# Performance work log

Hardware: AMD Instinct MI355X
Metric: run time of the kernel (lower is better)

## Reference

```python
import jax, jax.numpy as jnp
import numpy as np

B, S, D = 2, 2048, 2048
NQ, NKV = 32, 8
HD = D // NQ  # 64
THETA = 10000.0


def _rope_tables(seq_len, head_dim, theta):
    k = jnp.arange(0, head_dim, 2)[: head_dim // 2].astype(jnp.float32)
    inv_freq = 1.0 / (theta ** (k / head_dim))
    pos = jnp.arange(seq_len, dtype=jnp.float32)
    ang = pos[:, None] * inv_freq[None, :]          # [S, HD/2]
    ang = jnp.concatenate([ang, ang], axis=-1)       # [S, HD]
    return jnp.cos(ang), jnp.sin(ang)


def _apply_rope(x, cos, sin):
    # x: [B, H, S, HD]; cos/sin: [S, HD]
    h = x.shape[-1] // 2
    x1, x2 = x[..., :h], x[..., h:]
    rotated = jnp.concatenate([-x2, x1], axis=-1)
    return (x * cos[None, None] + rotated * sin[None, None]).astype(x.dtype)


def setup_inputs() -> dict:
    key = jax.random.key(0)
    ks = jax.random.split(key, 6)
    x = jax.random.normal(ks[0], (B, S, D), dtype=jnp.float32)
    attention_mask = jnp.ones((B, S), dtype=jnp.int32)
    Wq = jax.random.normal(ks[1], (NQ * HD, D), dtype=jnp.float32) * 0.02
    Wk = jax.random.normal(ks[2], (NKV * HD, D), dtype=jnp.float32) * 0.02
    Wv = jax.random.normal(ks[3], (NKV * HD, D), dtype=jnp.float32) * 0.02
    Wo = jax.random.normal(ks[4], (D, D), dtype=jnp.float32) * 0.02
    return {"x": x, "attention_mask": attention_mask,
            "Wq": Wq, "Wk": Wk, "Wv": Wv, "Wo": Wo}


def reference(x, attention_mask, Wq, Wk, Wv, Wo):
    b, s, d = x.shape
    # projections (nn.Linear: y = x @ W.T)
    q = jnp.einsum('bsd,od->bso', x, Wq).reshape(b, s, NQ, HD).transpose(0, 2, 1, 3)
    k = jnp.einsum('bsd,od->bso', x, Wk).reshape(b, s, NKV, HD).transpose(0, 2, 1, 3)
    v = jnp.einsum('bsd,od->bso', x, Wv).reshape(b, s, NKV, HD).transpose(0, 2, 1, 3)
    cos, sin = _rope_tables(s, HD, THETA)
    q = _apply_rope(q, cos, sin)
    k = _apply_rope(k, cos, sin)
    g = NQ // NKV
    k = jnp.repeat(k, g, axis=1)  # [b, NQ, s, HD]
    v = jnp.repeat(v, g, axis=1)
    attn = jnp.einsum('bhqd,bhkd->bhqk', q, k)
    causal = jnp.triu(jnp.ones((s, s), dtype=bool), k=1)
    attn = jnp.where(causal[None, None], -jnp.inf, attn)
    attn = jax.nn.softmax(attn / jnp.sqrt(jnp.float32(HD)), axis=-1)
    out = jnp.einsum('bhqk,bhkd->bhqd', attn, v)
    out = out.transpose(0, 2, 1, 3).reshape(b, s, d)
    return jnp.einsum('bsd,od->bso', out, Wo)
```

## Files before the change

kernel.cpp:

```cpp
#include <hip/hip_runtime.h>

#define B_   2
#define S_   2048
#define D_   2048
#define NQ_  32
#define NKV_ 8
#define HD_  64

typedef unsigned short u16;
typedef __bf16 bf16x8 __attribute__((ext_vector_type(8)));
typedef short  s16x4  __attribute__((ext_vector_type(4)));
typedef float  f32x4  __attribute__((ext_vector_type(4)));

#define GLB __attribute__((address_space(1)))
#define LDS __attribute__((address_space(3)))

__device__ inline u16 f2b(float f){
  union { float f; unsigned u; } v; v.f = f;
  unsigned r = (v.u + 0x7fffu + ((v.u >> 16) & 1u)) >> 16;
  return (u16)r;
}
__device__ inline float b2f(u16 b){
  union { unsigned u; float f; } v; v.u = ((unsigned)b) << 16;
  return v.f;
}

__device__ inline f32x4 mfma16(s16x4 a, s16x4 b, f32x4 c){
  return __builtin_amdgcn_mfma_f32_16x16x16bf16_1k(a, b, c, 0, 0, 0);
}

__device__ inline s16x4 pack4(float p0, float p1, float p2, float p3){
  union { float f; unsigned u; } a, b, c, d;
  a.f = p0; b.f = p1; c.f = p2; d.f = p3;
  union { uint2 u; s16x4 v; } r;
  r.u.x = (a.u >> 16) | (b.u & 0xffff0000u);
  r.u.y = (c.u >> 16) | (d.u & 0xffff0000u);
  return r.v;
}

__global__ void k_f2b_all(const float* __restrict__ x,  const float* __restrict__ wq,
                          const float* __restrict__ wk, const float* __restrict__ wv,
                          const float* __restrict__ wo,
                          u16* __restrict__ xb, u16* __restrict__ wqkvb, u16* __restrict__ wob){
  int i = blockIdx.x * blockDim.x + threadIdx.x;
  const float* src; u16* dst; int off;
  if (i < 2097152)      { src = x;  dst = xb;                  off = i; }
  else if (i < 3145728) { src = wq; dst = wqkvb;               off = i - 2097152; }
  else if (i < 3407872) { src = wk; dst = wqkvb + 2048*2048;   off = i - 3145728; }
  else if (i < 3670016) { src = wv; dst = wqkvb + 2560*2048;   off = i - 3407872; }
  else                  { src = wo; dst = wob;                 off = i - 3670016; }
  float4 f = ((const float4*)src)[off];
  uint2 pk;
  pk.x = (unsigned)f2b(f.x) | ((unsigned)f2b(f.y) << 16);
  pk.y = (unsigned)f2b(f.z) | ((unsigned)f2b(f.w) << 16);
  ((uint2*)dst)[off] = pk;
}

#define GEMM_CORE(K)                                                           \
  __shared__ __align__(16) u16 As[128*64];                                     \
  __shared__ __align__(16) u16 Bs[128*64];                                     \
  const int tid  = threadIdx.x;                                               \
  const int lane = tid & 63;                                                  \
  const int wave = tid >> 6;                                                  \
  const int wm = wave >> 1, wn = wave & 1;                                    \
  const int quad = lane >> 4, l16 = lane & 15;                                \
  const u16* Ab = A  + (size_t)blockIdx.y * 128 * (K);                        \
  const u16* Bb = Bm + (size_t)blockIdx.x * 128 * (K);                        \
  f32x4 acc[4][4];                                                            \
  for (int i = 0; i < 4; i++)                                                 \
    for (int j = 0; j < 4; j++) acc[i][j] = (f32x4){0.f, 0.f, 0.f, 0.f};      \
  const int R0 = wave * 32;                                                   \
  const int lr = lane >> 3;                                                   \
  const int gc = ((lane & 7) ^ lr) * 8;                                       \
  const int sk = l16 & 7;                                                     \
  for (int k0 = 0; k0 < (K); k0 += 64){                                       \
    __syncthreads();                                                          \
    _Pragma("unroll")                                                         \
    for (int m = 0; m < 4; m++){                                              \
      const u16* ga = Ab + (size_t)(R0 + m*8 + lr) * (K) + k0 + gc;           \
      const u16* gb = Bb + (size_t)(R0 + m*8 + lr) * (K) + k0 + gc;           \
      __builtin_amdgcn_global_load_lds((const GLB void*)ga, (LDS void*)&As[(R0 + m*8)*64], 16, 0, 0); \
      __builtin_amdgcn_global_load_lds((const GLB void*)gb, (LDS void*)&Bs[(R0 + m*8)*64], 16, 0, 0); \
    }                                                                          \
    __syncthreads();                                                          \
    bf16x8 af[4][2], bfr[4][2];                                               \
    _Pragma("unroll")                                                         \
    for (int i = 0; i < 4; i++)                                               \
      _Pragma("unroll")                                                       \
      for (int h = 0; h < 2; h++)                                             \
        af[i][h]  = *(const bf16x8*)&As[(wm*64 + i*16 + l16)*64 + (((h*4 + quad) ^ sk)*8)]; \
    _Pragma("unroll")                                                         \
    for (int j = 0; j < 4; j++)                                               \
      _Pragma("unroll")                                                       \
      for (int h = 0; h < 2; h++)                                             \
        bfr[j][h] = *(const bf16x8*)&Bs[(wn*64 + j*16 + l16)*64 + (((h*4 + quad) ^ sk)*8)]; \
    _Pragma("unroll")                                                         \
    for (int i = 0; i < 4; i++)                                               \
      _Pragma("unroll")                                                       \
      for (int j = 0; j < 4; j++){                                            \
        acc[i][j] = __builtin_amdgcn_mfma_f32_16x16x32_bf16(af[i][0], bfr[j][0], acc[i][j], 0, 0, 0); \
        acc[i][j] = __builtin_amdgcn_mfma_f32_16x16x32_bf16(af[i][1], bfr[j][1], acc[i][j], 0, 0, 0); \
      }                                                                        \
  }

#define QSCALE 0.18033688011112042f
__global__ __launch_bounds__(256, 3) void k_gemm_qkv(const u16* __restrict__ A,
                                                     const u16* __restrict__ Bm,
                                                     u16* __restrict__ qT,
                                                     u16* __restrict__ kT,
                                                     u16* __restrict__ vT){
  GEMM_CORE(2048)

  const int cb = blockIdx.x*128 + wn*64;

  if (cb < 2560){
    const bool isq = (cb < 2048);
    const int hh   = (isq ? cb : (cb - 2048)) >> 6;
    const int NH   = isq ? NQ_ : NKV_;
    u16* base      = isq ? qT : kT;
    const float sc = isq ? QSCALE : 1.0f;
    #pragma unroll
    for (int j = 0; j < 2; j++){
      const int d2 = j*16 + l16;
      const float invf = __expf(-(float)d2 * (9.210340371976184f / 32.0f));
      #pragma unroll
      for (int i = 0; i < 4; i++){
        const int row0 = blockIdx.y*128 + wm*64 + i*16 + quad*4;
        #pragma unroll
        for (int r = 0; r < 4; r++){
          const int row = row0 + r;
          const int s = row & (S_ - 1), b = row >> 11;
          float ang = (float)s * invf;
          float sn = __sinf(ang), cs = __cosf(ang);
          const float x1 = acc[i][j][r] * sc, x2 = acc[i][j+2][r] * sc;
          u16* drow = base + ((size_t)(b*NH + hh) * S_ + s) * 64;
          drow[d2]      = f2b(x1*cs - x2*sn);
          drow[d2 + 32] = f2b(x2*cs + x1*sn);
        }
      }
    }
  } else {
    const int fbase = cb - 2560;
    #pragma unroll
    for (int j = 0; j < 4; j++){
      const int f = fbase + j*16 + l16;
      const int kvh = f >> 6, d = f & 63;
      #pragma unroll
      for (int i = 0; i < 4; i++){
        const int row0 = blockIdx.y*128 + wm*64 + i*16 + quad*4;
        const int s0 = row0 & (S_ - 1), b = row0 >> 11;
        uint2 pk;
        pk.x = (unsigned)f2b(acc[i][j][0]) | ((unsigned)f2b(acc[i][j][1]) << 16);
        pk.y = (unsigned)f2b(acc[i][j][2]) | ((unsigned)f2b(acc[i][j][3]) << 16);
        *(uint2*)(vT + ((size_t)(b*NKV_ + kvh) * 64 + d) * S_ + s0) = pk;
      }
    }
  }
}

__global__ __launch_bounds__(256, 3) void k_gemm_bt(const u16* __restrict__ A,
                                                    const u16* __restrict__ Bm,
                                                    float* __restrict__ C,
                                                    int N){
  GEMM_CORE(2048)
  for (int i = 0; i < 4; i++){
    int row0 = blockIdx.y*128 + wm*64 + i*16 + quad*4;
    for (int j = 0; j < 4; j++){
      int col = blockIdx.x*128 + wn*64 + j*16 + l16;
      for (int r = 0; r < 4; r++)
        C[(size_t)(row0 + r) * N + col] = acc[i][j][r];
    }
  }
}

__global__ __launch_bounds__(256) void k_attn(const u16* __restrict__ qT,
                                              const u16* __restrict__ kT,
                                              const u16* __restrict__ vT,
                                              u16* __restrict__ P1,
                                              u16* __restrict__ P2,
                                              float* __restrict__ l1,
                                              float* __restrict__ l2){
  __shared__ __align__(16) u16 Ks[2][64*64];
  __shared__ __align__(16) u16 Vs[2][64*64];

  const int bid  = blockIdx.x;
  const int kvh  = bid & 7;
  const int b    = (bid >> 3) & 1;
  const int hq   = (bid >> 4) & 3;
  const int j    = bid >> 6;
  const int T    = 15 - (j >> 1);
  const int half = j & 1;
  const int h    = kvh*4 + hq;
  const int lane = threadIdx.x & 63, w = threadIdx.x >> 6;
  const int quad = lane >> 4, l16 = lane & 15;

  const u16* Qh = qT + (size_t)(b*NQ_ + h)    * S_ * 64;
  const u16* Kh = kT + (size_t)(b*NKV_ + kvh) * S_ * 64;
  const u16* Vh = vT + (size_t)(b*NKV_ + kvh) * 64 * S_;

  const int rr = lane >> 3;
  const int gg = (lane & 7) ^ rr;
  const int R  = w * 16;

  auto stage = [&](int c, int buf){
    const int kb = c * 64;
    const u16* gk0 = Kh + (size_t)(kb + R + rr)     * 64 + gg*8;
    const u16* gk1 = Kh + (size_t)(kb + R + 8 + rr) * 64 + gg*8;
    const u16* gv0 = Vh + (size_t)(R + rr)     * S_ + kb + gg*8;
    const u16* gv1 = Vh + (size_t)(R + 8 + rr) * S_ + kb + gg*8;
    __builtin_amdgcn_global_load_lds((const GLB void*)gk0, (LDS void*)&Ks[buf][R*64],     16, 0, 0);
    __builtin_amdgcn_global_load_lds((const GLB void*)gk1, (LDS void*)&Ks[buf][(R+8)*64], 16, 0, 0);
    __builtin_amdgcn_global_load_lds((const GLB void*)gv0, (LDS void*)&Vs[buf][R*64],     16, 0, 0);
    __builtin_amdgcn_global_load_lds((const GLB void*)gv1, (LDS void*)&Vs[buf][(R+8)*64], 16, 0, 0);
  };

  const int sw    = l16 & 7;
  const int koff0 = ((quad    ) ^ sw) * 8;
  const int koff1 = ((quad + 4) ^ sw) * 8;

  const int qb0 = 2*T, qb1 = 2*T + 1;
  const int qr0 = T*128 + w*16 + l16;
  const int qr1 = qr0 + 64;
  const int c0  = half ? (T + 1) : 0;
  const int nc  = T + 1;

  stage(c0, 0);

  bf16x8 qf[2][2];
  qf[0][0] = *(const bf16x8*)(Qh + (size_t)qr0*64 + quad*8);
  qf[0][1] = *(const bf16x8*)(Qh + (size_t)qr0*64 + 32 + quad*8);
  qf[1][0] = *(const bf16x8*)(Qh + (size_t)qr1*64 + quad*8);
  qf[1][1] = *(const bf16x8*)(Qh + (size_t)qr1*64 + 32 + quad*8);

  f32x4 o[2][4];
  #pragma unroll
  for (int s = 0; s < 2; s++)
    for (int dt = 0; dt < 4; dt++) o[s][dt] = (f32x4){0.f, 0.f, 0.f, 0.f};
  float lrow[2] = {0.f, 0.f};

  for (int i = 0; i < nc; i++){
    const int c = c0 + i;
    const int buf = i & 1;
    __syncthreads();
    if (i + 1 < nc) stage(c + 1, buf^1);

    const bool act0  = (c <= qb0);
    const bool diag0 = (c == qb0);
    const bool diag1 = (c == qb1);
    const u16* Kb = &Ks[buf][0];
    const u16* Vb = &Vs[buf][0];

    s16x4 pk[2][4];
    #pragma unroll
    for (int t = 0; t < 4; t++){
      const bool n0 = act0 && !(diag0 && t > w);
      const bool n1 = !(diag1 && t > w);
      if (!n0 && !n1) continue;
      const int rowb = (t*16 + l16)*64;
      bf16x8 ka0 = *(const bf16x8*)&Kb[rowb + koff0];
      bf16x8 ka1 = *(const bf16x8*)&Kb[rowb + koff1];
      #pragma unroll
      for (int s = 0; s < 2; s++){
        if (s == 0 ? !n0 : !n1) continue;
        f32x4 z = (f32x4){0.f, 0.f, 0.f, 0.f};
        z = __builtin_amdgcn_mfma_f32_16x16x32_bf16(ka0, qf[s][0], z, 0, 0, 0);
        z = __builtin_amdgcn_mfma_f32_16x16x32_bf16(ka1, qf[s][1], z, 0, 0, 0);
        if ((s == 0 ? diag0 : diag1) && t == w){
          #pragma unroll
          for (int r = 0; r < 4; r++)
            if (quad*4 + r > l16) z[r] = -1e30f;
        }
        float p0 = __builtin_amdgcn_exp2f(z[0]);
        float p1 = __builtin_amdgcn_exp2f(z[1]);
        float p2 = __builtin_amdgcn_exp2f(z[2]);
        float p3 = __builtin_amdgcn_exp2f(z[3]);
        lrow[s] += (p0 + p1) + (p2 + p3);
        pk[s][t] = pack4(p0, p1, p2, p3);
      }
    }

    #pragma unroll
    for (int dt = 0; dt < 4; dt++){
      const int rowb = (dt*16 + l16)*64;
      #pragma unroll
      for (int t = 0; t < 4; t++){
        const bool n0 = act0 && !(diag0 && t > w);
        const bool n1 = !(diag1 && t > w);
        if (!n0 && !n1) continue;
        const int vo = (((2*t + (quad >> 1)) ^ sw) * 8) + (quad & 1)*4;
        s16x4 va = *(const s16x4*)&Vb[rowb + vo];
        if (n0) o[0][dt] = mfma16(va, pk[0][t], o[0][dt]);
        if (n1) o[1][dt] = mfma16(va, pk[1][t], o[1][dt]);
      }
    }
  }

  u16*   Pd = half ? P2 : P1;
  float* ld = half ? l2 : l1;
  #pragma unroll
  for (int s = 0; s < 2; s++){
    float lsum = lrow[s];
    lsum += __shfl_xor(lsum, 16, 64);
    lsum += __shfl_xor(lsum, 32, 64);
    const int qrow = s ? qr1 : qr0;
    if (quad == 0) ld[(size_t)(b*S_ + qrow)*NQ_ + h] = lsum;
    u16* orow = Pd + (size_t)(b*S_ + qrow) * D_ + h*64;
    #pragma unroll
    for (int dt = 0; dt < 4; dt++){
      uint2 pkd;
      u16 e0 = f2b(o[s][dt][0]), e1 = f2b(o[s][dt][1]);
      u16 e2 = f2b(o[s][dt][2]), e3 = f2b(o[s][dt][3]);
      pkd.x = (unsigned)e0 | ((unsigned)e1 << 16);
      pkd.y = (unsigned)e2 | ((unsigned)e3 << 16);
      *(uint2*)(orow + dt*16 + quad*4) = pkd;
    }
  }
}

__global__ void k_combine(const u16* __restrict__ P1, const u16* __restrict__ P2,
                          const float* __restrict__ l1, const float* __restrict__ l2,
                          u16* __restrict__ out){
  int i = blockIdx.x * blockDim.x + threadIdx.x;
  int e = i << 2;
  int li = (e >> 11)*NQ_ + ((e >> 6) & 31);
  float inv = 1.0f / (l1[li] + l2[li]);
  uint2 a = *(const uint2*)(P1 + e);
  uint2 bq = *(const uint2*)(P2 + e);
  float o0 = (b2f(a.x & 0xffff)  + b2f(bq.x & 0xffff))  * inv;
  float o1 = (b2f(a.x >> 16)     + b2f(bq.x >> 16))     * inv;
  float o2 = (b2f(a.y & 0xffff)  + b2f(bq.y & 0xffff))  * inv;
  float o3 = (b2f(a.y >> 16)     + b2f(bq.y >> 16))     * inv;
  uint2 pk;
  pk.x = (unsigned)f2b(o0) | ((unsigned)f2b(o1) << 16);
  pk.y = (unsigned)f2b(o2) | ((unsigned)f2b(o3) << 16);
  *(uint2*)(out + e) = pk;
}

extern "C" void kernel_launch(void* const* d_in, const int* in_sizes, int n_in,
                              void* d_out, int out_size, void* d_ws, size_t ws_size,
                              hipStream_t stream){
  const float* x  = (const float*)d_in[0];
  const float* Wq = (const float*)d_in[2];
  const float* Wk = (const float*)d_in[3];
  const float* Wv = (const float*)d_in[4];
  const float* Wo = (const float*)d_in[5];

  char* ws = (char*)d_ws;
  u16*   xb    = (u16*)(ws);
  u16*   wqkvb = (u16*)(ws + 16777216);
  u16*   wob   = (u16*)(ws + 29360128);
  u16*   qTp   = (u16*)(ws + 37748736);
  u16*   kTp   = (u16*)(ws + 54525952);
  u16*   vTp   = (u16*)(ws + 58720256);
  u16*   P1    = xb;
  u16*   P2    = (u16*)(ws + 62914560);
  float* l1    = (float*)(ws + 79691776);
  float* l2    = (float*)(ws + 80216064);
  u16*   attnOut = qTp;

  k_f2b_all<<<dim3(18432), 256, 0, stream>>>(x, Wq, Wk, Wv, Wo, xb, wqkvb, wob);

  k_gemm_qkv<<<dim3(24, 32), 256, 0, stream>>>(xb, wqkvb, qTp, kTp, vTp);

  k_attn<<<dim3(2048), 256, 0, stream>>>(qTp, kTp, vTp, P1, P2, l1, l2);

  k_combine<<<dim3(8192), 256, 0, stream>>>(P1, P2, l1, l2, attnOut);

  k_gemm_bt<<<dim3(16, 32), 256, 0, stream>>>(attnOut, wob, (float*)d_out, 2048);
}
```

Before: 284.4 us.

## Balance causal attention work with table-driven KV splits and wider MFMA PV

```diff
diff --git a/kernel.cpp b/kernel.cpp
--- a/kernel.cpp
+++ b/kernel.cpp
@@ -25,16 +25,23 @@
   return v.f;
 }
 
-__device__ inline f32x4 mfma16(s16x4 a, s16x4 b, f32x4 c){
-  return __builtin_amdgcn_mfma_f32_16x16x16bf16_1k(a, b, c, 0, 0, 0);
-}
-
-__device__ inline s16x4 pack4(float p0, float p1, float p2, float p3){
-  union { float f; unsigned u; } a, b, c, d;
-  a.f = p0; b.f = p1; c.f = p2; d.f = p3;
+__device__ inline f32x4 mfma32(bf16x8 a, bf16x8 b, f32x4 c){
+  return __builtin_amdgcn_mfma_f32_16x16x32_bf16(a, b, c, 0, 0, 0);
+}
+
+__device__ inline bf16x8 cat8(s16x4 lo, s16x4 hi){
+  union { struct { s16x4 a, b; } s; bf16x8 v; } u;
+  u.s.a = lo; u.s.b = hi; return u.v;
+}
+
+__device__ inline s16x4 exppack(f32x4 z){
+  float p0 = __builtin_amdgcn_exp2f(z[0]);
+  float p1 = __builtin_amdgcn_exp2f(z[1]);
+  float p2 = __builtin_amdgcn_exp2f(z[2]);
+  float p3 = __builtin_amdgcn_exp2f(z[3]);
   union { uint2 u; s16x4 v; } r;
-  r.u.x = (a.u >> 16) | (b.u & 0xffff0000u);
-  r.u.y = (c.u >> 16) | (d.u & 0xffff0000u);
+  asm("v_cvt_pk_bf16_f32 %0, %1, %2" : "=v"(r.u.x) : "v"(p0), "v"(p1));
+  asm("v_cvt_pk_bf16_f32 %0, %1, %2" : "=v"(r.u.y) : "v"(p2), "v"(p3));
   return r.v;
 }
 
@@ -173,13 +180,34 @@
   }
 }
 
+__constant__ unsigned char JOB_T[40] = {
+  15,15,15,15,14,14,11,11,11,10, 7, 7, 3,
+  14,14,13,13,13,13,12,12,10,10, 9, 9, 6, 6,
+  12,12, 9, 8, 8, 8, 5, 5, 2,
+   4, 4, 1, 0};
+__constant__ unsigned char JOB_I[40] = {
+   0, 1, 2, 3, 1, 3, 0, 1, 2, 2, 0, 1, 0,
+   0, 2, 0, 1, 2, 3, 1, 3, 0, 1, 1, 2, 0, 1,
+   0, 2, 0, 0, 1, 2, 0, 1, 0,
+   0, 1, 0, 0};
+__constant__ unsigned char JOB_C0[40] = {
+   0, 8,16,24, 7,22, 0, 8,16,14, 0, 8, 0,
+   0,15, 0, 7,14,21, 6,19, 0, 7, 6,13, 0, 7,
+   0,13, 0, 0, 6,12, 0, 6, 0,
+   0, 5, 0, 0};
+__constant__ unsigned char JOB_NC[40] = {
+   8, 8, 8, 8, 8, 8, 8, 8, 8, 8, 8, 8, 8,
+   7, 7, 7, 7, 7, 7, 7, 7, 7, 7, 7, 7, 7, 7,
+   6, 6, 6, 6, 6, 6, 6, 6, 6,
+   5, 5, 4, 2};
+
 __global__ __launch_bounds__(256) void k_attn(const u16* __restrict__ qT,
                                               const u16* __restrict__ kT,
                                               const u16* __restrict__ vT,
-                                              u16* __restrict__ P1,
-                                              u16* __restrict__ P2,
-                                              float* __restrict__ l1,
-                                              float* __restrict__ l2){
+                                              u16* __restrict__ P1, u16* __restrict__ P2,
+                                              u16* __restrict__ P3, u16* __restrict__ P4,
+                                              float* __restrict__ l1, float* __restrict__ l2,
+                                              float* __restrict__ l3, float* __restrict__ l4){
   __shared__ __align__(16) u16 Ks[2][64*64];
   __shared__ __align__(16) u16 Vs[2][64*64];
 
@@ -188,8 +216,10 @@
   const int b    = (bid >> 3) & 1;
   const int hq   = (bid >> 4) & 3;
   const int j    = bid >> 6;
-  const int T    = 15 - (j >> 1);
-  const int half = j & 1;
+  const int T    = JOB_T[j];
+  const int slot = JOB_I[j];
+  const int c0   = JOB_C0[j];
+  const int nc   = JOB_NC[j];
   const int h    = kvh*4 + hq;
   const int lane = threadIdx.x & 63, w = threadIdx.x >> 6;
   const int quad = lane >> 4, l16 = lane & 15;
@@ -217,12 +247,15 @@
   const int sw    = l16 & 7;
   const int koff0 = ((quad    ) ^ sw) * 8;
   const int koff1 = ((quad + 4) ^ sw) * 8;
+  const int q2 = quad >> 1, q1 = (quad & 1) * 4;
+  const int vo00 = (((q2    ) ^ sw) * 8) + q1;
+  const int vo01 = (((q2 + 2) ^ sw) * 8) + q1;
+  const int vo10 = (((q2 + 4) ^ sw) * 8) + q1;
+  const int vo11 = (((q2 + 6) ^ sw) * 8) + q1;
 
   const int qb0 = 2*T, qb1 = 2*T + 1;
   const int qr0 = T*128 + w*16 + l16;
   const int qr1 = qr0 + 64;
-  const int c0  = half ? (T + 1) : 0;
-  const int nc  = T + 1;
 
   stage(c0, 0);
 
@@ -236,7 +269,11 @@
   #pragma unroll
   for (int s = 0; s < 2; s++)
     for (int dt = 0; dt < 4; dt++) o[s][dt] = (f32x4){0.f, 0.f, 0.f, 0.f};
-  float lrow[2] = {0.f, 0.f};
+  f32x4 os0 = (f32x4){0.f,0.f,0.f,0.f}, os1 = (f32x4){0.f,0.f,0.f,0.f};
+  union { unsigned u[4]; bf16x8 v; } onesu;
+  onesu.u[0] = onesu.u[1] = onesu.u[2] = onesu.u[3] = 0x3F803F80u;
+  const bf16x8 ones = onesu.v;
+  const s16x4 z4 = {0,0,0,0};
 
   for (int i = 0; i < nc; i++){
     const int c = c0 + i;
@@ -250,61 +287,77 @@
     const u16* Kb = &Ks[buf][0];
     const u16* Vb = &Vs[buf][0];
 
-    s16x4 pk[2][4];
+    s16x4 pk0[4], pk1[4];
     #pragma unroll
     for (int t = 0; t < 4; t++){
-      const bool n0 = act0 && !(diag0 && t > w);
-      const bool n1 = !(diag1 && t > w);
-      if (!n0 && !n1) continue;
-      const int rowb = (t*16 + l16)*64;
-      bf16x8 ka0 = *(const bf16x8*)&Kb[rowb + koff0];
-      bf16x8 ka1 = *(const bf16x8*)&Kb[rowb + koff1];
-      #pragma unroll
-      for (int s = 0; s < 2; s++){
-        if (s == 0 ? !n0 : !n1) continue;
-        f32x4 z = (f32x4){0.f, 0.f, 0.f, 0.f};
-        z = __builtin_amdgcn_mfma_f32_16x16x32_bf16(ka0, qf[s][0], z, 0, 0, 0);
-        z = __builtin_amdgcn_mfma_f32_16x16x32_bf16(ka1, qf[s][1], z, 0, 0, 0);
-        if ((s == 0 ? diag0 : diag1) && t == w){
-          #pragma unroll
-          for (int r = 0; r < 4; r++)
-            if (quad*4 + r > l16) z[r] = -1e30f;
-        }
-        float p0 = __builtin_amdgcn_exp2f(z[0]);
-        float p1 = __builtin_amdgcn_exp2f(z[1]);
-        float p2 = __builtin_amdgcn_exp2f(z[2]);
-        float p3 = __builtin_amdgcn_exp2f(z[3]);
-        lrow[s] += (p0 + p1) + (p2 + p3);
-        pk[s][t] = pack4(p0, p1, p2, p3);
-      }
-    }
+      const bool need0 = act0 && !(diag0 && t > w);
+      const bool need1 = !(diag1 && t > w);
+      if (need0 || need1){
+        const int rowb = (t*16 + l16)*64;
+        bf16x8 ka0 = *(const bf16x8*)&Kb[rowb + koff0];
+        bf16x8 ka1 = *(const bf16x8*)&Kb[rowb + koff1];
+        if (need0){
+          f32x4 z = (f32x4){0.f, 0.f, 0.f, 0.f};
+          z = mfma32(ka0, qf[0][0], z);
+          z = mfma32(ka1, qf[0][1], z);
+          if (diag0 && t == w){
+            #pragma unroll
+            for (int r = 0; r < 4; r++)
+              if (quad*4 + r > l16) z[r] = -1e30f;
+          }
+          pk0[t] = exppack(z);
+        } else pk0[t] = z4;
+        if (need1){
+          f32x4 z = (f32x4){0.f, 0.f, 0.f, 0.f};
+          z = mfma32(ka0, qf[1][0], z);
+          z = mfma32(ka1, qf[1][1], z);
+          if (diag1 && t == w){
+            #pragma unroll
+            for (int r = 0; r < 4; r++)
+              if (quad*4 + r > l16) z[r] = -1e30f;
+          }
+          pk1[t] = exppack(z);
+        } else pk1[t] = z4;
+      } else { pk0[t] = z4; pk1[t] = z4; }
+    }
+
+    bf16x8 pb00 = cat8(pk0[0], pk0[1]), pb01 = cat8(pk0[2], pk0[3]);
+    bf16x8 pb10 = cat8(pk1[0], pk1[1]), pb11 = cat8(pk1[2], pk1[3]);
+
+    if (act0){
+      os0 = mfma32(ones, pb00, os0);
+      os0 = mfma32(ones, pb01, os0);
+    }
+    os1 = mfma32(ones, pb10, os1);
+    os1 = mfma32(ones, pb11, os1);
 
     #pragma unroll
     for (int dt = 0; dt < 4; dt++){
       const int rowb = (dt*16 + l16)*64;
-      #pragma unroll
-      for (int t = 0; t < 4; t++){
-        const bool n0 = act0 && !(diag0 && t > w);
-        const bool n1 = !(diag1 && t > w);
-        if (!n0 && !n1) continue;
-        const int vo = (((2*t + (quad >> 1)) ^ sw) * 8) + (quad & 1)*4;
-        s16x4 va = *(const s16x4*)&Vb[rowb + vo];
-        if (n0) o[0][dt] = mfma16(va, pk[0][t], o[0][dt]);
-        if (n1) o[1][dt] = mfma16(va, pk[1][t], o[1][dt]);
+      bf16x8 va0 = cat8(*(const s16x4*)&Vb[rowb + vo00], *(const s16x4*)&Vb[rowb + vo01]);
+      bf16x8 va1 = cat8(*(const s16x4*)&Vb[rowb + vo10], *(const s16x4*)&Vb[rowb + vo11]);
+      if (act0){
+        o[0][dt] = mfma32(va0, pb00, o[0][dt]);
+        o[0][dt] = mfma32(va1, pb01, o[0][dt]);
       }
-    }
-  }
-
-  u16*   Pd = half ? P2 : P1;
-  float* ld = half ? l2 : l1;
+      o[1][dt] = mfma32(va0, pb10, o[1][dt]);
+      o[1][dt] = mfma32(va1, pb11, o[1][dt]);
+    }
+  }
+
+  u16* Pd; float* ld; int rowoff;
+  if      (slot == 0){ Pd = P1; ld = l1; rowoff = b*2048; }
+  else if (slot == 1){ Pd = P2; ld = l2; rowoff = b*2048; }
+  else if (slot == 2){ Pd = P3; ld = l3; rowoff = b*1024 - 1024; }
+  else               { Pd = P4; ld = l4; rowoff = b*512  - 1536; }
+
   #pragma unroll
   for (int s = 0; s < 2; s++){
-    float lsum = lrow[s];
-    lsum += __shfl_xor(lsum, 16, 64);
-    lsum += __shfl_xor(lsum, 32, 64);
     const int qrow = s ? qr1 : qr0;
-    if (quad == 0) ld[(size_t)(b*S_ + qrow)*NQ_ + h] = lsum;
-    u16* orow = Pd + (size_t)(b*S_ + qrow) * D_ + h*64;
+    const int prow = rowoff + qrow;
+    const f32x4 osv = s ? os1 : os0;
+    if (quad == 0) ld[(size_t)prow * NQ_ + h] = osv[0];
+    u16* orow = Pd + (size_t)prow * D_ + h*64;
     #pragma unroll
     for (int dt = 0; dt < 4; dt++){
       uint2 pkd;
@@ -318,21 +371,47 @@
 }
 
 __global__ void k_combine(const u16* __restrict__ P1, const u16* __restrict__ P2,
+                          const u16* __restrict__ P3, const u16* __restrict__ P4,
                           const float* __restrict__ l1, const float* __restrict__ l2,
+                          const float* __restrict__ l3, const float* __restrict__ l4,
                           u16* __restrict__ out){
   int i = blockIdx.x * blockDim.x + threadIdx.x;
   int e = i << 2;
-  int li = (e >> 11)*NQ_ + ((e >> 6) & 31);
-  float inv = 1.0f / (l1[li] + l2[li]);
+  int qrowb = e >> 11;
+  int qrow  = qrowb & 2047;
+  int b     = qrowb >> 11;
+  int h     = (e >> 6) & 31;
+  int T     = qrow >> 7;
+  int li    = qrowb * NQ_ + h;
+
+  float lsum = l1[li];
   uint2 a = *(const uint2*)(P1 + e);
-  uint2 bq = *(const uint2*)(P2 + e);
-  float o0 = (b2f(a.x & 0xffff)  + b2f(bq.x & 0xffff))  * inv;
-  float o1 = (b2f(a.x >> 16)     + b2f(bq.x >> 16))     * inv;
-  float o2 = (b2f(a.y & 0xffff)  + b2f(bq.y & 0xffff))  * inv;
-  float o3 = (b2f(a.y >> 16)     + b2f(bq.y >> 16))     * inv;
+  float o0 = b2f(a.x & 0xffff), o1 = b2f(a.x >> 16);
+  float o2 = b2f(a.y & 0xffff), o3 = b2f(a.y >> 16);
+  if (T >= 4){
+    lsum += l2[li];
+    uint2 p = *(const uint2*)(P2 + e);
+    o0 += b2f(p.x & 0xffff); o1 += b2f(p.x >> 16);
+    o2 += b2f(p.y & 0xffff); o3 += b2f(p.y >> 16);
+  }
+  if (T >= 8){
+    int r3 = (b << 10) + qrow - 1024;
+    lsum += l3[r3 * NQ_ + h];
+    uint2 p = *(const uint2*)(P3 + (((size_t)r3) << 11) + (e & 2047));
+    o0 += b2f(p.x & 0xffff); o1 += b2f(p.x >> 16);
+    o2 += b2f(p.y & 0xffff); o3 += b2f(p.y >> 16);
+  }
+  if (T >= 12){
+    int r4 = (b << 9) + qrow - 1536;
+    lsum += l4[r4 * NQ_ + h];
+    uint2 p = *(const uint2*)(P4 + (((size_t)r4) << 11) + (e & 2047));
+    o0 += b2f(p.x & 0xffff); o1 += b2f(p.x >> 16);
+    o2 += b2f(p.y & 0xffff); o3 += b2f(p.y >> 16);
+  }
+  float inv = 1.0f / lsum;
   uint2 pk;
-  pk.x = (unsigned)f2b(o0) | ((unsigned)f2b(o1) << 16);
-  pk.y = (unsigned)f2b(o2) | ((unsigned)f2b(o3) << 16);
+  pk.x = (unsigned)f2b(o0 * inv) | ((unsigned)f2b(o1 * inv) << 16);
+  pk.y = (unsigned)f2b(o2 * inv) | ((unsigned)f2b(o3 * inv) << 16);
   *(uint2*)(out + e) = pk;
 }
 
@@ -354,17 +433,21 @@
   u16*   vTp   = (u16*)(ws + 58720256);
   u16*   P1    = xb;
   u16*   P2    = (u16*)(ws + 62914560);
+  u16*   P3    = (u16*)(ws + 16777216);
+  u16*   P4    = (u16*)(ws + 25165824);
   float* l1    = (float*)(ws + 79691776);
   float* l2    = (float*)(ws + 80216064);
+  float* l3    = (float*)d_out;
+  float* l4    = (float*)((char*)d_out + 262144);
   u16*   attnOut = qTp;
 
   k_f2b_all<<<dim3(18432), 256, 0, stream>>>(x, Wq, Wk, Wv, Wo, xb, wqkvb, wob);
 
   k_gemm_qkv<<<dim3(24, 32), 256, 0, stream>>>(xb, wqkvb, qTp, kTp, vTp);
 
-  k_attn<<<dim3(2048), 256, 0, stream>>>(qTp, kTp, vTp, P1, P2, l1, l2);
-
-  k_combine<<<dim3(8192), 256, 0, stream>>>(P1, P2, l1, l2, attnOut);
+  k_attn<<<dim3(2560), 256, 0, stream>>>(qTp, kTp, vTp, P1, P2, P3, P4, l1, l2, l3, l4);
+
+  k_combine<<<dim3(8192), 256, 0, stream>>>(P1, P2, P3, P4, l1, l2, l3, l4, attnOut);
 
   k_gemm_bt<<<dim3(16, 32), 256, 0, stream>>>(attnOut, wob, (float*)d_out, 2048);
 }
```

After: 284.0 us. No clear change (-0.1%).
